# Performance work log

Measured on AMD Instinct MI355X. Metric: run time of the kernel, lower is better.

The kernel has to match this reference:

```python
import jax, jax.numpy as jnp
import numpy as np

WS = 8          # window_size
H = 4           # num_heads
C = 128         # embed_dim
D = C // H      # head_dim
L = WS * WS     # tokens per window
B = 4096        # batch * num_windows


def _make_rel_index(ws):
    coords = np.stack(np.meshgrid(np.arange(ws), np.arange(ws), indexing='ij'))  # [2,ws,ws]
    flat = coords.reshape(2, -1)                       # [2, L]
    rel = flat[:, :, None] - flat[:, None, :]          # [2, L, L]
    rel = rel.transpose(1, 2, 0) + ws - 1              # [L, L, 2]
    return (rel[..., 0] * (2 * ws - 1) + rel[..., 1]).astype(np.int32)  # [L, L]


def setup_inputs() -> dict:
    key = jax.random.key(0)
    ks = jax.random.split(key, 10)
    s = 0.02
    return {
        'query': jax.random.normal(ks[0], (B, L, C), jnp.float32),
        'Wq': jax.random.normal(ks[1], (C, C), jnp.float32) * s,
        'bq': jnp.zeros((C,), jnp.float32),
        'Wk': jax.random.normal(ks[2], (C, C), jnp.float32) * s,
        'bk': jnp.zeros((C,), jnp.float32),
        'Wv': jax.random.normal(ks[3], (C, C), jnp.float32) * s,
        'bv': jnp.zeros((C,), jnp.float32),
        'Wo': jax.random.normal(ks[4], (C, C), jnp.float32) * s,
        'bo': jnp.zeros((C,), jnp.float32),
        'bias_table': jax.random.normal(ks[5], ((2 * WS - 1) ** 2, H), jnp.float32) * s,
        'rel_index': jnp.asarray(_make_rel_index(WS)),
    }


def reference(query, Wq, bq, Wk, bk, Wv, bv, Wo, bo, bias_table, rel_index):
    scale = D ** -0.5
    # projections (torch Linear: x @ W.T + b)
    q = (query @ Wq.T + bq).reshape(B, L, H, D).transpose(0, 2, 1, 3)  # [B,H,L,D]
    k = (query @ Wk.T + bk).reshape(B, L, H, D).transpose(0, 2, 1, 3)
    v = (query @ Wv.T + bv).reshape(B, L, H, D).transpose(0, 2, 1, 3)
    attn = jnp.einsum('bhqd,bhkd->bhqk', q, k) * scale               # [B,H,L,L]
    bias = bias_table[rel_index]                                      # [L,L,H]
    attn = attn + bias.transpose(2, 0, 1)[None]                       # add RPB
    attn = jax.nn.softmax(attn, axis=-1)
    out = jnp.einsum('bhqk,bhkd->bqhd', attn, v).reshape(B, L, C)
    out = out @ Wo.T + bo
    return out
```

## Files before the change

### kernel.cpp

```cpp
#include <hip/hip_runtime.h>
#include <hip/hip_bf16.h>

typedef unsigned int u32;
typedef unsigned short u16;
typedef __attribute__((ext_vector_type(8))) short bf16x8;
typedef __attribute__((ext_vector_type(4))) float f32x4;
typedef __attribute__((ext_vector_type(2))) u32 u32x2;

#define LOG2E 1.4426950408889634f
#define SCALE 0.17677669529663687f

__device__ __forceinline__ u16 f2bf(float f) {
    return __builtin_bit_cast(u16, __float2bfloat16(f));
}
__device__ __forceinline__ u32 pkbf(float a, float b) {
    return (u32)f2bf(a) | ((u32)f2bf(b) << 16);
}

__device__ __forceinline__ int sw128(int r, int e) { return r * 128 + (e ^ ((r & 7) << 3)); }
__device__ __forceinline__ int sw64 (int r, int e) { return r * 64  + (e ^ ((r & 7) << 3)); }

__global__ __launch_bounds__(256) void prep_kernel(
    const float* __restrict__ Wq, const float* __restrict__ Wk,
    const float* __restrict__ Wv, const float* __restrict__ Wo,
    const float* __restrict__ bias_table, const int* __restrict__ rel_index,
    u16* __restrict__ wsW, float* __restrict__ wsB)
{
    int idx = blockIdx.x * 256 + threadIdx.x;
    if (idx < 16384) {
        wsW[idx]         = f2bf(Wq[idx] * (SCALE * LOG2E));
        wsW[16384 + idx] = f2bf(Wk[idx]);
        wsW[32768 + idx] = f2bf(Wv[idx]);
        wsW[49152 + idx] = f2bf(Wo[idx]);
        int h = idx >> 12, t = (idx >> 8) & 15, l = (idx >> 2) & 63, r = idx & 3;
        int mt = t >> 2, nt = t & 3, g = l >> 4, c = l & 15;
        int kk = 16 * mt + 4 * g + r, q = 16 * nt + c;
        wsB[idx] = bias_table[rel_index[q * 64 + kk] * 4 + h] * LOG2E;
    }
}

__global__ __launch_bounds__(256, 3) void wattn_kernel(
    const float* __restrict__ x,
    const float* __restrict__ bq, const float* __restrict__ bk,
    const float* __restrict__ bv, const float* __restrict__ bo,
    const u16* __restrict__ Wbf, const float* __restrict__ biasT,
    float* __restrict__ out)
{
    __shared__ u16 smem[24576];

    const int b    = blockIdx.x;
    const int tid  = threadIdx.x;
    const int wid  = tid >> 6;
    const int lane = tid & 63;
    const int g    = lane >> 4;
    const int c    = lane & 15;
    const int h    = wid;

    u16* Xs = smem;
    u16* qk = smem + wid * 6144;
    u16* vT = qk + 4096;

    {
        const float* xb = x + (size_t)b * 8192;
        #pragma unroll
        for (int it = 0; it < 8; ++it) {
            int idx = it * 1024 + tid * 4;
            f32x4 v = __builtin_nontemporal_load((const f32x4*)(xb + idx));
            int row = idx >> 7, col = idx & 127;
            u32x2 wv;
            wv.x = pkbf(v[0], v[1]);
            wv.y = pkbf(v[2], v[3]);
            *(u32x2*)&Xs[sw128(row, col)] = wv;
        }
    }
    __syncthreads();

    bf16x8 xa[4][4];
    #pragma unroll
    for (int mt = 0; mt < 4; ++mt)
        #pragma unroll
        for (int kt = 0; kt < 4; ++kt)
            xa[mt][kt] = *(const bf16x8*)&Xs[sw128(16 * mt + c, 32 * kt + 8 * g)];
    __syncthreads();

    #pragma unroll
    for (int p = 0; p < 3; ++p) {
        const float* bp = (p == 0) ? bq : (p == 1) ? bk : bv;
        #pragma unroll
        for (int j = 0; j < 2; ++j) {
            int nt = 2 * h + j;
            float bcol = bp[16 * nt + c];
            if (p == 0) bcol *= (SCALE * LOG2E);
            f32x4 acc[4];
            #pragma unroll
            for (int mt = 0; mt < 4; ++mt) { f32x4 t = {bcol, bcol, bcol, bcol}; acc[mt] = t; }
            const u16* W = Wbf + p * 16384 + (16 * nt + c) * 128;
            #pragma unroll
            for (int kt = 0; kt < 4; ++kt) {
                bf16x8 bfr = *(const bf16x8*)(W + 32 * kt + 8 * g);
                #pragma unroll
                for (int mt = 0; mt < 4; ++mt)
                    acc[mt] = __builtin_amdgcn_mfma_f32_16x16x32_bf16(xa[mt][kt], bfr, acc[mt], 0, 0, 0);
            }
            if (p < 2) {
                int colb = p * 32 + 16 * j + c;
                #pragma unroll
                for (int mt = 0; mt < 4; ++mt)
                    #pragma unroll
                    for (int r = 0; r < 4; ++r)
                        qk[sw64(16 * mt + 4 * g + r, colb)] = f2bf(acc[mt][r]);
            } else {
                #pragma unroll
                for (int mt = 0; mt < 4; ++mt) {
                    u32x2 wv;
                    wv.x = pkbf(acc[mt][0], acc[mt][1]);
                    wv.y = pkbf(acc[mt][2], acc[mt][3]);
                    *(u32x2*)&vT[sw64(16 * j + c, 16 * mt + 4 * g)] = wv;
                }
            }
        }
    }

    bf16x8 ka[4], qb[4];
    #pragma unroll
    for (int t = 0; t < 4; ++t) {
        qb[t] = *(const bf16x8*)&qk[sw64(16 * t + c, 8 * g)];
        ka[t] = *(const bf16x8*)&qk[sw64(16 * t + c, 32 + 8 * g)];
    }
    f32x4 accS[4][4];
    const f32x4* bT = (const f32x4*)(biasT + h * 4096);
    #pragma unroll
    for (int mt = 0; mt < 4; ++mt)
        #pragma unroll
        for (int nt = 0; nt < 4; ++nt)
            accS[mt][nt] = __builtin_amdgcn_mfma_f32_16x16x32_bf16(
                ka[mt], qb[nt], bT[(mt * 4 + nt) * 64 + lane], 0, 0, 0);

    float rinv[4];
    #pragma unroll
    for (int nt = 0; nt < 4; ++nt) {
        float m = accS[0][nt][0];
        #pragma unroll
        for (int mt = 0; mt < 4; ++mt)
            #pragma unroll
            for (int r = 0; r < 4; ++r) m = fmaxf(m, accS[mt][nt][r]);
        m = fmaxf(m, __shfl_xor(m, 16, 64));
        m = fmaxf(m, __shfl_xor(m, 32, 64));
        float s = 0.f;
        #pragma unroll
        for (int mt = 0; mt < 4; ++mt)
            #pragma unroll
            for (int r = 0; r < 4; ++r) {
                float e = exp2f(accS[mt][nt][r] - m);
                accS[mt][nt][r] = e;
                s += e;
            }
        s += __shfl_xor(s, 16, 64);
        s += __shfl_xor(s, 32, 64);
        rinv[nt] = 1.0f / s;
    }

    #pragma unroll
    for (int mt = 0; mt < 4; ++mt)
        #pragma unroll
        for (int nt = 0; nt < 4; ++nt) {
            u32x2 wv;
            wv.x = pkbf(accS[mt][nt][0], accS[mt][nt][1]);
            wv.y = pkbf(accS[mt][nt][2], accS[mt][nt][3]);
            *(u32x2*)&qk[sw64(16 * nt + c, 16 * mt + 4 * g)] = wv;
        }

    f32x4 accO[2][4];
    #pragma unroll
    for (int mD = 0; mD < 2; ++mD)
        #pragma unroll
        for (int nt = 0; nt < 4; ++nt) { f32x4 z = {0.f, 0.f, 0.f, 0.f}; accO[mD][nt] = z; }
    #pragma unroll
    for (int kt = 0; kt < 2; ++kt) {
        bf16x8 va[2];
        #pragma unroll
        for (int mD = 0; mD < 2; ++mD)
            va[mD] = *(const bf16x8*)&vT[sw64(16 * mD + c, 32 * kt + 8 * g)];
        #pragma unroll
        for (int nt = 0; nt < 4; ++nt) {
            bf16x8 pb = *(const bf16x8*)&qk[sw64(16 * nt + c, 32 * kt + 8 * g)];
            #pragma unroll
            for (int mD = 0; mD < 2; ++mD)
                accO[mD][nt] = __builtin_amdgcn_mfma_f32_16x16x32_bf16(va[mD], pb, accO[mD][nt], 0, 0, 0);
        }
    }
    __syncthreads();

    #pragma unroll
    for (int mD = 0; mD < 2; ++mD)
        #pragma unroll
        for (int nt = 0; nt < 4; ++nt) {
            float riv = rinv[nt];
            u32x2 wv;
            wv.x = pkbf(accO[mD][nt][0] * riv, accO[mD][nt][1] * riv);
            wv.y = pkbf(accO[mD][nt][2] * riv, accO[mD][nt][3] * riv);
            *(u32x2*)&Xs[sw128(16 * nt + c, 32 * h + 16 * mD + 4 * g)] = wv;
        }
    __syncthreads();

    bf16x8 ha[4][4];
    #pragma unroll
    for (int mt = 0; mt < 4; ++mt)
        #pragma unroll
        for (int kt = 0; kt < 4; ++kt)
            ha[mt][kt] = *(const bf16x8*)&Xs[sw128(16 * mt + c, 32 * kt + 8 * g)];
    const u16* Wo_ = Wbf + 49152;
    float* ob = out + (size_t)b * 8192;
    #pragma unroll
    for (int j = 0; j < 2; ++j) {
        int OT = 2 * wid + j;
        float bocol = bo[16 * OT + c];
        f32x4 acc[4];
        #pragma unroll
        for (int mt = 0; mt < 4; ++mt) { f32x4 t = {bocol, bocol, bocol, bocol}; acc[mt] = t; }
        const u16* W = Wo_ + (16 * OT + c) * 128;
        #pragma unroll
        for (int kt = 0; kt < 4; ++kt) {
            bf16x8 wf = *(const bf16x8*)(W + 32 * kt + 8 * g);
            #pragma unroll
            for (int mt = 0; mt < 4; ++mt)
                acc[mt] = __builtin_amdgcn_mfma_f32_16x16x32_bf16(ha[mt][kt], wf, acc[mt], 0, 0, 0);
        }
        #pragma unroll
        for (int mt = 0; mt < 4; ++mt)
            #pragma unroll
            for (int r = 0; r < 4; ++r)
                __builtin_nontemporal_store(acc[mt][r],
                    &ob[(16 * mt + 4 * g + r) * 128 + 16 * OT + c]);
    }
}

extern "C" void kernel_launch(void* const* d_in, const int* in_sizes, int n_in,
                              void* d_out, int out_size, void* d_ws, size_t ws_size,
                              hipStream_t stream)
{
    const float* query      = (const float*)d_in[0];
    const float* Wq         = (const float*)d_in[1];
    const float* bq         = (const float*)d_in[2];
    const float* Wk         = (const float*)d_in[3];
    const float* bk         = (const float*)d_in[4];
    const float* Wv         = (const float*)d_in[5];
    const float* bv         = (const float*)d_in[6];
    const float* Wo         = (const float*)d_in[7];
    const float* bo         = (const float*)d_in[8];
    const float* bias_table = (const float*)d_in[9];
    const int*   rel_index  = (const int*)d_in[10];

    u16*   wsW = (u16*)d_ws;
    float* wsB = (float*)((char*)d_ws + 131072);

    prep_kernel<<<dim3(64), dim3(256), 0, stream>>>(Wq, Wk, Wv, Wo, bias_table, rel_index, wsW, wsB);
    wattn_kernel<<<dim3(4096), dim3(256), 0, stream>>>(query, bq, bk, bv, bo, wsW, wsB, (float*)d_out);
}
```

Before: 127.3 us.

## Keep Q/K/V/P in registers via MFMA layout tricks, shrink LDS for occupancy

Reorders the Q/K projections (weights as A operand, X as B) so the accumulator layout can be packed straight into MFMA operand fragments. This removes the per-wave LDS round trips for Q, K, V and the softmax probabilities. Shared memory drops from 48KB to 16KB and launch bounds rise to 4 blocks per CU to raise occupancy. The cost is more register pressure, V projection reading X from LDS again, and normalising probabilities before the bf16 cast instead of after PV, which slightly changes rounding.

```diff
diff --git a/kernel.cpp b/kernel.cpp
--- a/kernel.cpp
+++ b/kernel.cpp
@@ -6,6 +6,7 @@
 typedef __attribute__((ext_vector_type(8))) short bf16x8;
 typedef __attribute__((ext_vector_type(4))) float f32x4;
 typedef __attribute__((ext_vector_type(2))) u32 u32x2;
+typedef __attribute__((ext_vector_type(4))) u32 u32x4;
 
 #define LOG2E 1.4426950408889634f
 #define SCALE 0.17677669529663687f
@@ -16,9 +17,12 @@
 __device__ __forceinline__ u32 pkbf(float a, float b) {
     return (u32)f2bf(a) | ((u32)f2bf(b) << 16);
 }
+__device__ __forceinline__ bf16x8 pk8(f32x4 a, f32x4 b) {
+    u32x4 p = {pkbf(a[0], a[1]), pkbf(a[2], a[3]), pkbf(b[0], b[1]), pkbf(b[2], b[3])};
+    return __builtin_bit_cast(bf16x8, p);
+}
 
 __device__ __forceinline__ int sw128(int r, int e) { return r * 128 + (e ^ ((r & 7) << 3)); }
-__device__ __forceinline__ int sw64 (int r, int e) { return r * 64  + (e ^ ((r & 7) << 3)); }
 
 __global__ __launch_bounds__(256) void prep_kernel(
     const float* __restrict__ Wq, const float* __restrict__ Wk,
@@ -39,14 +43,14 @@
     }
 }
 
-__global__ __launch_bounds__(256, 3) void wattn_kernel(
+__global__ __launch_bounds__(256, 4) void wattn_kernel(
     const float* __restrict__ x,
     const float* __restrict__ bq, const float* __restrict__ bk,
     const float* __restrict__ bv, const float* __restrict__ bo,
     const u16* __restrict__ Wbf, const float* __restrict__ biasT,
     float* __restrict__ out)
 {
-    __shared__ u16 smem[24576];
+    __shared__ u16 smem[8192];
 
     const int b    = blockIdx.x;
     const int tid  = threadIdx.x;
@@ -57,8 +61,6 @@
     const int h    = wid;
 
     u16* Xs = smem;
-    u16* qk = smem + wid * 6144;
-    u16* vT = qk + 4096;
 
     {
         const float* xb = x + (size_t)b * 8192;
@@ -75,68 +77,52 @@
     }
     __syncthreads();
 
-    bf16x8 xa[4][4];
-    #pragma unroll
-    for (int mt = 0; mt < 4; ++mt)
-        #pragma unroll
-        for (int kt = 0; kt < 4; ++kt)
-            xa[mt][kt] = *(const bf16x8*)&Xs[sw128(16 * mt + c, 32 * kt + 8 * g)];
-    __syncthreads();
-
-    #pragma unroll
-    for (int p = 0; p < 3; ++p) {
-        const float* bp = (p == 0) ? bq : (p == 1) ? bk : bv;
-        #pragma unroll
-        for (int j = 0; j < 2; ++j) {
-            int nt = 2 * h + j;
-            float bcol = bp[16 * nt + c];
-            if (p == 0) bcol *= (SCALE * LOG2E);
-            f32x4 acc[4];
-            #pragma unroll
-            for (int mt = 0; mt < 4; ++mt) { f32x4 t = {bcol, bcol, bcol, bcol}; acc[mt] = t; }
-            const u16* W = Wbf + p * 16384 + (16 * nt + c) * 128;
-            #pragma unroll
-            for (int kt = 0; kt < 4; ++kt) {
-                bf16x8 bfr = *(const bf16x8*)(W + 32 * kt + 8 * g);
-                #pragma unroll
-                for (int mt = 0; mt < 4; ++mt)
-                    acc[mt] = __builtin_amdgcn_mfma_f32_16x16x32_bf16(xa[mt][kt], bfr, acc[mt], 0, 0, 0);
+    f32x4 accQ[2][4], accK[2][4];
+    #pragma unroll
+    for (int CT = 0; CT < 2; ++CT) {
+        float4 bbq = *(const float4*)&bq[32 * h + 16 * CT + 4 * g];
+        float4 bbk = *(const float4*)&bk[32 * h + 16 * CT + 4 * g];
+        f32x4 qi = {bbq.x * (SCALE * LOG2E), bbq.y * (SCALE * LOG2E),
+                    bbq.z * (SCALE * LOG2E), bbq.w * (SCALE * LOG2E)};
+        f32x4 ki = {bbk.x, bbk.y, bbk.z, bbk.w};
+        #pragma unroll
+        for (int nt = 0; nt < 4; ++nt) { accQ[CT][nt] = qi; accK[CT][nt] = ki; }
+    }
+    #pragma unroll
+    for (int kt = 0; kt < 4; ++kt) {
+        bf16x8 xt[4];
+        #pragma unroll
+        for (int nt = 0; nt < 4; ++nt)
+            xt[nt] = *(const bf16x8*)&Xs[sw128(16 * nt + c, 32 * kt + 8 * g)];
+        #pragma unroll
+        for (int CT = 0; CT < 2; ++CT) {
+            bf16x8 wq = *(const bf16x8*)(Wbf + (32 * h + 16 * CT + c) * 128 + 32 * kt + 8 * g);
+            bf16x8 wk = *(const bf16x8*)(Wbf + 16384 + (32 * h + 16 * CT + c) * 128 + 32 * kt + 8 * g);
+            #pragma unroll
+            for (int nt = 0; nt < 4; ++nt) {
+                accQ[CT][nt] = __builtin_amdgcn_mfma_f32_16x16x32_bf16(wq, xt[nt], accQ[CT][nt], 0, 0, 0);
+                accK[CT][nt] = __builtin_amdgcn_mfma_f32_16x16x32_bf16(wk, xt[nt], accK[CT][nt], 0, 0, 0);
             }
-            if (p < 2) {
-                int colb = p * 32 + 16 * j + c;
-                #pragma unroll
-                for (int mt = 0; mt < 4; ++mt)
-                    #pragma unroll
-                    for (int r = 0; r < 4; ++r)
-                        qk[sw64(16 * mt + 4 * g + r, colb)] = f2bf(acc[mt][r]);
-            } else {
-                #pragma unroll
-                for (int mt = 0; mt < 4; ++mt) {
-                    u32x2 wv;
-                    wv.x = pkbf(acc[mt][0], acc[mt][1]);
-                    wv.y = pkbf(acc[mt][2], acc[mt][3]);
-                    *(u32x2*)&vT[sw64(16 * j + c, 16 * mt + 4 * g)] = wv;
-                }
-            }
-        }
-    }
-
-    bf16x8 ka[4], qb[4];
-    #pragma unroll
-    for (int t = 0; t < 4; ++t) {
-        qb[t] = *(const bf16x8*)&qk[sw64(16 * t + c, 8 * g)];
-        ka[t] = *(const bf16x8*)&qk[sw64(16 * t + c, 32 + 8 * g)];
-    }
+        }
+    }
+    bf16x8 qf8[4], kf8[4];
+    #pragma unroll
+    for (int nt = 0; nt < 4; ++nt) {
+        qf8[nt] = pk8(accQ[0][nt], accQ[1][nt]);
+        kf8[nt] = pk8(accK[0][nt], accK[1][nt]);
+    }
+
     f32x4 accS[4][4];
-    const f32x4* bT = (const f32x4*)(biasT + h * 4096);
-    #pragma unroll
-    for (int mt = 0; mt < 4; ++mt)
-        #pragma unroll
-        for (int nt = 0; nt < 4; ++nt)
-            accS[mt][nt] = __builtin_amdgcn_mfma_f32_16x16x32_bf16(
-                ka[mt], qb[nt], bT[(mt * 4 + nt) * 64 + lane], 0, 0, 0);
-
-    float rinv[4];
+    {
+        const f32x4* bT = (const f32x4*)(biasT + h * 4096);
+        #pragma unroll
+        for (int mt = 0; mt < 4; ++mt)
+            #pragma unroll
+            for (int nt = 0; nt < 4; ++nt)
+                accS[mt][nt] = __builtin_amdgcn_mfma_f32_16x16x32_bf16(
+                    kf8[mt], qf8[nt], bT[(mt * 4 + nt) * 64 + lane], 0, 0, 0);
+    }
+
     #pragma unroll
     for (int nt = 0; nt < 4; ++nt) {
         float m = accS[0][nt][0];
@@ -157,50 +143,71 @@
             }
         s += __shfl_xor(s, 16, 64);
         s += __shfl_xor(s, 32, 64);
-        rinv[nt] = 1.0f / s;
-    }
-
-    #pragma unroll
-    for (int mt = 0; mt < 4; ++mt)
-        #pragma unroll
-        for (int nt = 0; nt < 4; ++nt) {
-            u32x2 wv;
-            wv.x = pkbf(accS[mt][nt][0], accS[mt][nt][1]);
-            wv.y = pkbf(accS[mt][nt][2], accS[mt][nt][3]);
-            *(u32x2*)&qk[sw64(16 * nt + c, 16 * mt + 4 * g)] = wv;
-        }
-
-    f32x4 accO[2][4];
-    #pragma unroll
-    for (int mD = 0; mD < 2; ++mD)
-        #pragma unroll
-        for (int nt = 0; nt < 4; ++nt) { f32x4 z = {0.f, 0.f, 0.f, 0.f}; accO[mD][nt] = z; }
-    #pragma unroll
-    for (int kt = 0; kt < 2; ++kt) {
-        bf16x8 va[2];
-        #pragma unroll
-        for (int mD = 0; mD < 2; ++mD)
-            va[mD] = *(const bf16x8*)&vT[sw64(16 * mD + c, 32 * kt + 8 * g)];
-        #pragma unroll
-        for (int nt = 0; nt < 4; ++nt) {
-            bf16x8 pb = *(const bf16x8*)&qk[sw64(16 * nt + c, 32 * kt + 8 * g)];
-            #pragma unroll
-            for (int mD = 0; mD < 2; ++mD)
-                accO[mD][nt] = __builtin_amdgcn_mfma_f32_16x16x32_bf16(va[mD], pb, accO[mD][nt], 0, 0, 0);
-        }
-    }
+        float rinv = 1.0f / s;
+        #pragma unroll
+        for (int mt = 0; mt < 4; ++mt)
+            #pragma unroll
+            for (int r = 0; r < 4; ++r) accS[mt][nt][r] *= rinv;
+    }
+    bf16x8 pf8[2][4];
+    #pragma unroll
+    for (int u = 0; u < 2; ++u)
+        #pragma unroll
+        for (int nt = 0; nt < 4; ++nt)
+            pf8[u][nt] = pk8(accS[2 * u][nt], accS[2 * u + 1][nt]);
+
+    f32x4 vacc[2][4];
+    #pragma unroll
+    for (int j = 0; j < 2; ++j) {
+        float bc = bv[32 * h + 16 * j + c];
+        f32x4 bi = {bc, bc, bc, bc};
+        #pragma unroll
+        for (int mt = 0; mt < 4; ++mt) vacc[j][mt] = bi;
+    }
+    #pragma unroll
+    for (int kt = 0; kt < 4; ++kt) {
+        bf16x8 xt[4];
+        #pragma unroll
+        for (int mt = 0; mt < 4; ++mt)
+            xt[mt] = *(const bf16x8*)&Xs[sw128(16 * mt + c, 32 * kt + 8 * g)];
+        #pragma unroll
+        for (int j = 0; j < 2; ++j) {
+            bf16x8 wv = *(const bf16x8*)(Wbf + 32768 + (32 * h + 16 * j + c) * 128 + 32 * kt + 8 * g);
+            #pragma unroll
+            for (int mt = 0; mt < 4; ++mt)
+                vacc[j][mt] = __builtin_amdgcn_mfma_f32_16x16x32_bf16(xt[mt], wv, vacc[j][mt], 0, 0, 0);
+        }
+    }
+    bf16x8 vf8[2][2];
+    #pragma unroll
+    for (int j = 0; j < 2; ++j)
+        #pragma unroll
+        for (int u = 0; u < 2; ++u)
+            vf8[j][u] = pk8(vacc[j][2 * u], vacc[j][2 * u + 1]);
+
+    f32x4 accO[4][2];
+    #pragma unroll
+    for (int nt = 0; nt < 4; ++nt)
+        #pragma unroll
+        for (int j = 0; j < 2; ++j) { f32x4 z = {0.f, 0.f, 0.f, 0.f}; accO[nt][j] = z; }
+    #pragma unroll
+    for (int u = 0; u < 2; ++u)
+        #pragma unroll
+        for (int nt = 0; nt < 4; ++nt)
+            #pragma unroll
+            for (int j = 0; j < 2; ++j)
+                accO[nt][j] = __builtin_amdgcn_mfma_f32_16x16x32_bf16(
+                    pf8[u][nt], vf8[j][u], accO[nt][j], 0, 0, 0);
+
     __syncthreads();
 
     #pragma unroll
-    for (int mD = 0; mD < 2; ++mD)
-        #pragma unroll
-        for (int nt = 0; nt < 4; ++nt) {
-            float riv = rinv[nt];
-            u32x2 wv;
-            wv.x = pkbf(accO[mD][nt][0] * riv, accO[mD][nt][1] * riv);
-            wv.y = pkbf(accO[mD][nt][2] * riv, accO[mD][nt][3] * riv);
-            *(u32x2*)&Xs[sw128(16 * nt + c, 32 * h + 16 * mD + 4 * g)] = wv;
-        }
+    for (int nt = 0; nt < 4; ++nt)
+        #pragma unroll
+        for (int j = 0; j < 2; ++j)
+            #pragma unroll
+            for (int r = 0; r < 4; ++r)
+                Xs[sw128(16 * nt + 4 * g + r, 32 * h + 16 * j + c)] = f2bf(accO[nt][j][r]);
     __syncthreads();
 
     bf16x8 ha[4][4];
```

Result: slower. 215.0 us (+68.9%).
